# Optimization experiments

Measured on AMD Instinct MI355X. Metric: run time of the kernel, lower is better.

Reference implementation:

```python
import jax, jax.numpy as jnp
import numpy as np

B, L, D = 8, 2048, 64
EPS = 1e-8


def setup_inputs() -> dict:
    key = jax.random.key(0)
    ks = jax.random.split(key, 7)
    s = 1.0 / np.sqrt(D)  # ~ torch Linear default init scale
    return {
        "x": jax.random.normal(ks[0], (B, L, D), dtype=jnp.float32),
        "B_w": jax.random.normal(ks[1], (D, D), dtype=jnp.float32) * s,
        "B_b": jax.random.normal(ks[2], (D,), dtype=jnp.float32) * s,
        "C_w": jax.random.normal(ks[3], (D, D), dtype=jnp.float32) * s,
        "C_b": jax.random.normal(ks[4], (D,), dtype=jnp.float32) * s,
        "V_w": jax.random.normal(ks[5], (D, D), dtype=jnp.float32) * s,
        "V_b": jax.random.normal(ks[6], (D,), dtype=jnp.float32) * s,
    }


def reference(x, B_w, B_b, C_w, C_b, V_w, V_b):
    # torch nn.Linear: y = x @ W.T + b
    BZ = jnp.einsum('bld,ed->ble', x, B_w) + B_b   # (B,L,D)
    CZ = jnp.einsum('bld,ed->ble', x, C_w) + C_b   # (B,L,D)
    scores = jnp.einsum('bld,bmd->blm', BZ, CZ)     # (B,L,L)
    attn = jax.nn.relu(scores)
    # note: normalization over dim=-2 (column sums), as in the original
    attn = attn / (attn.sum(axis=-2, keepdims=True) + EPS)
    VZ = jnp.einsum('bld,ed->ble', x, V_w) + V_b   # (B,L,D)
    out = jnp.einsum('blm,bmd->bld', attn, VZ)      # (B,L,D)
    return x + out
```

## Files before the change

### kernel.cpp

```cpp
#include <hip/hip_runtime.h>

typedef unsigned short u16;
typedef unsigned int u32;
typedef __bf16 bf16x8 __attribute__((ext_vector_type(8)));
typedef float f32x16 __attribute__((ext_vector_type(16)));
typedef const void __attribute__((address_space(1))) gvoid;
typedef void __attribute__((address_space(3))) lvoid;

#define GLOAD16(gp, lp) __builtin_amdgcn_global_load_lds((gvoid*)(gp), (lvoid*)(lp), 16, 0, 0)
#define POST_BARRIER_FENCE() do { __builtin_amdgcn_sched_barrier(0); asm volatile("" ::: "memory"); } while (0)

namespace {
constexpr int Ln = 2048;
constexpr float EPS = 1e-8f;
}

__device__ __forceinline__ u32 pk2(float lo, float hi) {
    u32 r;
    asm("v_cvt_pk_bf16_f32 %0, %1, %2" : "=v"(r) : "v"(lo), "v"(hi));
    return r;
}

__device__ __forceinline__ void half_swap(u32 a, u32 b, u32& na, u32& nb) {
    u32 sa = (u32)__shfl_xor((int)a, 32, 64);
    u32 sb = (u32)__shfl_xor((int)b, 32, 64);
    int hi = (threadIdx.x & 63) >> 5;
    na = hi ? a : sb;
    nb = hi ? sa : b;
}

__global__ __launch_bounds__(128) void proj_k(
    const float* __restrict__ x,
    const float* __restrict__ Bw, const float* __restrict__ Bb,
    const float* __restrict__ Cw, const float* __restrict__ Cb,
    const float* __restrict__ Vw, const float* __restrict__ Vb,
    u16* __restrict__ BZh, u16* __restrict__ CZh, u16* __restrict__ VZTh)
{
    const int tid = threadIdx.x;
    const int ln = tid & 31;
    const int g5 = (tid >> 5) & 1;
    const int w  = tid >> 6;
    const int row0 = blockIdx.x * 64 + w * 32;

    bf16x8 wf[3][2][4];
    const float* const Wp[3] = {Bw, Cw, Vw};
    #pragma unroll
    for (int m = 0; m < 3; ++m)
      #pragma unroll
      for (int e = 0; e < 2; ++e)
        #pragma unroll
        for (int c = 0; c < 4; ++c) {
            const float* p = Wp[m] + (e * 32 + ln) * 64 + c * 16 + g5 * 8;
            const float4 lo = *(const float4*)p;
            const float4 hi = *(const float4*)(p + 4);
            uint4 t4;
            t4.x = pk2(lo.x, lo.y); t4.y = pk2(lo.z, lo.w);
            t4.z = pk2(hi.x, hi.y); t4.w = pk2(hi.z, hi.w);
            wf[m][e][c] = __builtin_bit_cast(bf16x8, t4);
        }
    bf16x8 xf[4];
    {
        const float* xp = x + (row0 + ln) * 64 + g5 * 8;
        #pragma unroll
        for (int c = 0; c < 4; ++c) {
            const float4 lo = *(const float4*)(xp + c * 16);
            const float4 hi = *(const float4*)(xp + c * 16 + 4);
            uint4 t4;
            t4.x = pk2(lo.x, lo.y); t4.y = pk2(lo.z, lo.w);
            t4.z = pk2(hi.x, hi.y); t4.w = pk2(hi.z, hi.w);
            xf[c] = __builtin_bit_cast(bf16x8, t4);
        }
    }
    const int b   = row0 >> 11;
    const int l0b = row0 & 2047;
    const float* const biasBC[2] = {Bb, Cb};
    u16* const outBC[2] = {BZh, CZh};
    #pragma unroll
    for (int m = 0; m < 2; ++m) {
        #pragma unroll
        for (int e = 0; e < 2; ++e) {
            f32x16 st;
            #pragma unroll
            for (int q = 0; q < 4; ++q) {
                const float4 bv = *(const float4*)(biasBC[m] + e * 32 + q * 8 + g5 * 4);
                st[q*4+0] = bv.x; st[q*4+1] = bv.y; st[q*4+2] = bv.z; st[q*4+3] = bv.w;
            }
            #pragma unroll
            for (int c = 0; c < 4; ++c)
                st = __builtin_amdgcn_mfma_f32_32x32x16_bf16(wf[m][e][c], xf[c], st, 0, 0, 0);
            u16* op = outBC[m] + (row0 + ln) * 64 + e * 32 + g5 * 4;
            #pragma unroll
            for (int q = 0; q < 4; ++q) {
                uint2 pk;
                pk.x = pk2(st[q*4+0], st[q*4+1]);
                pk.y = pk2(st[q*4+2], st[q*4+3]);
                *(uint2*)(op + q * 8) = pk;
            }
        }
    }
    #pragma unroll
    for (int e = 0; e < 2; ++e) {
        const float vb = Vb[e * 32 + ln];
        f32x16 st;
        #pragma unroll
        for (int r = 0; r < 16; ++r) st[r] = vb;
        #pragma unroll
        for (int c = 0; c < 4; ++c)
            st = __builtin_amdgcn_mfma_f32_32x32x16_bf16(xf[c], wf[2][e][c], st, 0, 0, 0);
        u16* op = VZTh + (b * 64 + e * 32 + ln) * Ln + l0b + g5 * 4;
        #pragma unroll
        for (int q = 0; q < 4; ++q) {
            uint2 pk;
            pk.x = pk2(st[q*4+0], st[q*4+1]);
            pk.y = pk2(st[q*4+2], st[q*4+3]);
            *(uint2*)(op + q * 8) = pk;
        }
    }
}

__global__ __launch_bounds__(512) void denom_k(
    const u16* __restrict__ BZh, const u16* __restrict__ CZh,
    float* __restrict__ denp)
{
    __shared__ __attribute__((aligned(16))) char smem2[49152 + 1024];
    float* const red = (float*)(smem2 + 49152);
    const int tid = threadIdx.x;
    const int lane = tid & 63;
    const int ln = lane & 31;
    const int g5 = lane >> 5;
    const int w = tid >> 6;
    const int wm2 = w & 1, wl2 = w >> 1;
    const int flat = (int)blockIdx.z * 256 + (int)blockIdx.y * 32 + (int)blockIdx.x;
    const int nf = (flat & 7) * 64 + (flat >> 3);
    const int b = nf >> 6;
    const int rem = nf & 63;
    const int mb = (rem & 31) * 64;
    const int half = rem >> 5;
    const int l0h = half * 1024;
    const int wave_base = tid & ~63;

    bf16x8 af[4];
    {
        const u16* cp = CZh + ((b * Ln + mb + wm2 * 32 + ln) << 6) + g5 * 8;
        #pragma unroll
        for (int c = 0; c < 4; ++c) af[c] = *(const bf16x8*)(cp + c * 16);
    }
    auto stageD = [&](int t) {
        char* buf = smem2 + (t % 3) * 16384;
        #pragma unroll
        for (int it = 0; it < 2; ++it) {
            int j = (it << 9) + tid;
            int r = j >> 3;
            int u = (j & 7) ^ (r & 7);
            GLOAD16(BZh + ((b * Ln + l0h + t * 128 + r) << 6) + (u << 3),
                    buf + ((it << 9) + wave_base) * 16);
        }
    };
    stageD(0); stageD(1);
    __syncthreads();
    float accs[16];
    #pragma unroll
    for (int r = 0; r < 16; ++r) accs[r] = 0.f;
    const int lr = wl2 * 32 + ln;
    for (int t = 0; t < 8; ++t) {
        if (t > 0) {
            if (t < 7) asm volatile("s_waitcnt vmcnt(2)" ::: "memory");
            else       asm volatile("s_waitcnt vmcnt(0)" ::: "memory");
            __builtin_amdgcn_s_barrier();
            POST_BARRIER_FENCE();
        }
        if (t + 2 < 8) stageD(t + 2);
        const char* buf = smem2 + (t % 3) * 16384;
        f32x16 st = {};
        __builtin_amdgcn_s_setprio(1);
        #pragma unroll
        for (int c = 0; c < 4; ++c) {
            int un = (c << 1) | g5;
            bf16x8 bfr = *(const bf16x8*)(buf + (lr << 7) + ((un ^ (lr & 7)) << 4));
            st = __builtin_amdgcn_mfma_f32_32x32x16_bf16(af[c], bfr, st, 0, 0, 0);
        }
        __builtin_amdgcn_s_setprio(0);
        #pragma unroll
        for (int r = 0; r < 16; ++r) accs[r] += fmaxf(st[r], 0.f);
    }
    #pragma unroll
    for (int msk = 1; msk <= 16; msk <<= 1)
        #pragma unroll
        for (int r = 0; r < 16; ++r)
            accs[r] += __shfl_xor(accs[r], msk, 64);
    if (ln == 0) {
        #pragma unroll
        for (int r = 0; r < 16; ++r) {
            int mloc = wm2 * 32 + (r & 3) + ((r >> 2) << 3) + g5 * 4;
            red[mloc * 4 + wl2] = accs[r];
        }
    }
    __syncthreads();
    if (tid < 64)
        denp[(half * 8 + b) * Ln + mb + tid] =
            red[tid*4+0] + red[tid*4+1] + red[tid*4+2] + red[tid*4+3];
}

__global__ __launch_bounds__(512) void fused_out(
    const float* __restrict__ x,
    const u16* __restrict__ BZh, const u16* __restrict__ CZh,
    const u16* __restrict__ VZTh, const float* __restrict__ denp,
    float* __restrict__ out)
{
    __shared__ __attribute__((aligned(16))) char smem[57344];
    float* const denl = (float*)smem;
    char* const bufs = smem + 8192;
    const int tid = threadIdx.x;
    const int lane = tid & 63;
    const int ln = lane & 31;
    const int g5 = lane >> 5;
    const int w = tid >> 6;
    const int wm = w & 3;
    const int wl = w >> 2;
    const int bx = (int)blockIdx.x;
    const int nf = (bx & 7) * 32 + (bx >> 3);
    const int b = nf >> 5;
    const int l0 = (nf & 31) * 64;
    const int wave_base = tid & ~63;

    auto stage = [&](int t) {
        char* vzb = bufs + (t % 3) * 16384;
        #pragma unroll
        for (int it = 0; it < 2; ++it) {
            int j = (it << 9) + tid;
            int r = j >> 4;
            int uu = (j & 15) ^ (r & 7);
            GLOAD16(VZTh + ((b << 6) + r) * Ln + (t << 7) + (uu << 3),
                    vzb + ((it << 9) + wave_base) * 16);
        }
    };
    const u16* const cp0 = CZh + ((b * Ln + wm * 32 + ln) << 6) + g5 * 8;
    auto loadA = [&](int t, bf16x8* dst) {
        const u16* p = cp0 + ((t * 128) << 6);
        #pragma unroll
        for (int c = 0; c < 4; ++c) dst[c] = *(const bf16x8*)(p + c * 16);
    };

    {
        const float4 c0 = *(const float4*)(denp + b * Ln + tid * 4);
        const float4 c1 = *(const float4*)(denp + (8 + b) * Ln + tid * 4);
        float4 dv;
        dv.x = 1.f / (c0.x + c1.x + EPS);
        dv.y = 1.f / (c0.y + c1.y + EPS);
        dv.z = 1.f / (c0.z + c1.z + EPS);
        dv.w = 1.f / (c0.w + c1.w + EPS);
        *(float4*)(denl + tid * 4) = dv;
    }
    bf16x8 bzf[4];
    {
        const u16* bp = BZh + ((b * Ln + l0 + wl * 32 + ln) << 6) + g5 * 8;
        #pragma unroll
        for (int c = 0; c < 4; ++c) bzf[c] = *(const bf16x8*)(bp + c * 16);
    }
    stage(0); stage(1);
    bf16x8 aF[2][4];
    loadA(0, aF[0]);
    __syncthreads();

    f32x16 acc0 = {}, acc1 = {};
    #pragma unroll
    for (int t = 0; t < 16; ++t) {
        const int cur = t & 1;
        if (t > 0) {
            __builtin_amdgcn_s_barrier();
            POST_BARRIER_FENCE();
        }
        if (t + 2 < 16) stage(t + 2);
        if (t + 1 < 16) loadA(t + 1, aF[cur ^ 1]);
        f32x16 st = {};
        __builtin_amdgcn_s_setprio(1);
        #pragma unroll
        for (int c = 0; c < 4; ++c)
            st = __builtin_amdgcn_mfma_f32_32x32x16_bf16(aF[cur][c], bzf[c], st, 0, 0, 0);
        __builtin_amdgcn_s_setprio(0);
        const int mq0 = (t << 7) + wm * 32;
        u32 wv[8];
        #pragma unroll
        for (int q = 0; q < 4; ++q) {
            const float4 dq = *(const float4*)(denl + mq0 + q * 8 + g5 * 4);
            float p0 = fmaxf(st[q*4+0], 0.f) * dq.x;
            float p1 = fmaxf(st[q*4+1], 0.f) * dq.y;
            float p2 = fmaxf(st[q*4+2], 0.f) * dq.z;
            float p3 = fmaxf(st[q*4+3], 0.f) * dq.w;
            wv[q*2+0] = pk2(p0, p1);
            wv[q*2+1] = pk2(p2, p3);
        }
        u32 f0w0, f0w1, f0w2, f0w3, f1w0, f1w1, f1w2, f1w3;
        half_swap(wv[2], wv[0], f0w2, f0w0);
        half_swap(wv[3], wv[1], f0w3, f0w1);
        half_swap(wv[6], wv[4], f1w2, f1w0);
        half_swap(wv[7], wv[5], f1w3, f1w1);
        bf16x8 pf0, pf1;
        { uint4 t4; t4.x=f0w0; t4.y=f0w1; t4.z=f0w2; t4.w=f0w3; pf0 = __builtin_bit_cast(bf16x8, t4); }
        { uint4 t4; t4.x=f1w0; t4.y=f1w1; t4.z=f1w2; t4.w=f1w3; pf1 = __builtin_bit_cast(bf16x8, t4); }
        const char* vz = bufs + (t % 3) * 16384;
        const int un00 = (wm << 2) | g5;
        const int un01 = (wm << 2) | 2 | g5;
        __builtin_amdgcn_s_setprio(1);
        {
            bf16x8 av;
            av = *(const bf16x8*)(vz + (ln << 8) + ((un00 ^ (ln & 7)) << 4));
            acc0 = __builtin_amdgcn_mfma_f32_32x32x16_bf16(av, pf0, acc0, 0, 0, 0);
            av = *(const bf16x8*)(vz + (ln << 8) + ((un01 ^ (ln & 7)) << 4));
            acc0 = __builtin_amdgcn_mfma_f32_32x32x16_bf16(av, pf1, acc0, 0, 0, 0);
            av = *(const bf16x8*)(vz + ((32 + ln) << 8) + ((un00 ^ (ln & 7)) << 4));
            acc1 = __builtin_amdgcn_mfma_f32_32x32x16_bf16(av, pf0, acc1, 0, 0, 0);
            av = *(const bf16x8*)(vz + ((32 + ln) << 8) + ((un01 ^ (ln & 7)) << 4));
            acc1 = __builtin_amdgcn_mfma_f32_32x32x16_bf16(av, pf1, acc1, 0, 0, 0);
        }
        __builtin_amdgcn_s_setprio(0);
    }

    __syncthreads();
    float* red = (float*)smem;
    constexpr int LSTR = 36;
    constexpr int SSTR = 64 * LSTR;
    if (wm != 0) {
        float* base = red + ((wm - 1) * 2 + wl) * SSTR + lane * LSTR;
        #pragma unroll
        for (int r = 0; r < 16; ++r) { base[r] = acc0[r]; base[16 + r] = acc1[r]; }
    }
    __syncthreads();
    if (wm == 0) {
        #pragma unroll
        for (int s = 0; s < 3; ++s) {
            float* base = red + (s * 2 + wl) * SSTR + lane * LSTR;
            #pragma unroll
            for (int r = 0; r < 16; ++r) { acc0[r] += base[r]; acc1[r] += base[16 + r]; }
        }
        const int row = b * Ln + l0 + wl * 32 + ln;
        #pragma unroll
        for (int q = 0; q < 4; ++q) {
            const int d0 = q * 8 + g5 * 4;
            const float4 x0 = *(const float4*)(x + row * 64 + d0);
            float4 o0;
            o0.x = x0.x + acc0[q*4+0]; o0.y = x0.y + acc0[q*4+1];
            o0.z = x0.z + acc0[q*4+2]; o0.w = x0.w + acc0[q*4+3];
            *(float4*)(out + row * 64 + d0) = o0;
            const float4 x1 = *(const float4*)(x + row * 64 + 32 + d0);
            float4 o1;
            o1.x = x1.x + acc1[q*4+0]; o1.y = x1.y + acc1[q*4+1];
            o1.z = x1.z + acc1[q*4+2]; o1.w = x1.w + acc1[q*4+3];
            *(float4*)(out + row * 64 + 32 + d0) = o1;
        }
    }
}

extern "C" void kernel_launch(void* const* d_in, const int* in_sizes, int n_in,
                              void* d_out, int out_size, void* d_ws, size_t ws_size,
                              hipStream_t stream) {
    const float* x  = (const float*)d_in[0];
    const float* Bw = (const float*)d_in[1];
    const float* Bb = (const float*)d_in[2];
    const float* Cw = (const float*)d_in[3];
    const float* Cb = (const float*)d_in[4];
    const float* Vw = (const float*)d_in[5];
    const float* Vb = (const float*)d_in[6];
    float* out = (float*)d_out;
    char* wsb = (char*)d_ws;
    u16* BZh  = (u16*)wsb;
    u16* CZh  = (u16*)(wsb + (2u << 20));
    u16* VZTh = (u16*)(wsb + (4u << 20));
    float* denp = (float*)(wsb + (6u << 20));

    proj_k<<<dim3(256), 128, 0, stream>>>(x, Bw, Bb, Cw, Cb, Vw, Vb, BZh, CZh, VZTh);
    denom_k<<<dim3(32, 8, 2), 512, 0, stream>>>(BZh, CZh, denp);
    fused_out<<<dim3(256), 512, 0, stream>>>(x, BZh, CZh, VZTh, denp, out);
}
```

Before: 56.57 us.

## Restructure fused_out to stage CZ and VZ via LDS in 256-wide m tiles

The fused output kernel now has each of 8 waves own a 32-row m slice and all 64 l rows, instead of splitting waves over l halves and m quarters. CZ tiles are now staged into LDS with async global-to-LDS loads alongside VZ, double-buffered in 256-column chunks, which halves the loop trips and reuses each CZ fragment for two score tiles. The cross-wave reduction becomes a three-step tree over 8 waves, and proj_k is relaunched as 128 blocks of 256 threads. This raises LDS use to about 136KB per block, which limits occupancy to one block per CU, and adds a full vmcnt wait before each barrier.

```diff
diff --git a/kernel.cpp b/kernel.cpp
--- a/kernel.cpp
+++ b/kernel.cpp
@@ -29,7 +29,7 @@
     nb = hi ? sa : b;
 }
 
-__global__ __launch_bounds__(128) void proj_k(
+__global__ __launch_bounds__(256) void proj_k(
     const float* __restrict__ x,
     const float* __restrict__ Bw, const float* __restrict__ Bb,
     const float* __restrict__ Cw, const float* __restrict__ Cb,
@@ -40,7 +40,7 @@
     const int ln = tid & 31;
     const int g5 = (tid >> 5) & 1;
     const int w  = tid >> 6;
-    const int row0 = blockIdx.x * 64 + w * 32;
+    const int row0 = blockIdx.x * 128 + w * 32;
 
     bf16x8 wf[3][2][4];
     const float* const Wp[3] = {Bw, Cw, Vw};
@@ -207,16 +207,14 @@
     const u16* __restrict__ VZTh, const float* __restrict__ denp,
     float* __restrict__ out)
 {
-    __shared__ __attribute__((aligned(16))) char smem[57344];
+    __shared__ __attribute__((aligned(16))) char smem[139264];
     float* const denl = (float*)smem;
     char* const bufs = smem + 8192;
     const int tid = threadIdx.x;
     const int lane = tid & 63;
     const int ln = lane & 31;
     const int g5 = lane >> 5;
-    const int w = tid >> 6;
-    const int wm = w & 3;
-    const int wl = w >> 2;
+    const int wm = tid >> 6;
     const int bx = (int)blockIdx.x;
     const int nf = (bx & 7) * 32 + (bx >> 3);
     const int b = nf >> 5;
@@ -224,23 +222,28 @@
     const int wave_base = tid & ~63;
 
     auto stage = [&](int t) {
-        char* vzb = bufs + (t % 3) * 16384;
-        #pragma unroll
-        for (int it = 0; it < 2; ++it) {
+        char* czb = bufs + (t & 1) * 65536;
+        char* vzb = czb + 32768;
+        const int m0s = t << 8;
+        #pragma unroll
+        for (int it = 0; it < 4; ++it) {
             int j = (it << 9) + tid;
-            int r = j >> 4;
-            int uu = (j & 15) ^ (r & 7);
-            GLOAD16(VZTh + ((b << 6) + r) * Ln + (t << 7) + (uu << 3),
+            int r = j >> 3;
+            int u = (j & 7) ^ (r & 7);
+            GLOAD16(CZh + ((b * Ln + m0s + r) << 6) + (u << 3),
+                    czb + ((it << 9) + wave_base) * 16);
+        }
+        #pragma unroll
+        for (int it = 0; it < 4; ++it) {
+            int j = (it << 9) + tid;
+            int r = j >> 5;
+            int u = (j & 31) ^ (r & 7);
+            GLOAD16(VZTh + ((b << 6) + r) * Ln + m0s + (u << 3),
                     vzb + ((it << 9) + wave_base) * 16);
         }
     };
-    const u16* const cp0 = CZh + ((b * Ln + wm * 32 + ln) << 6) + g5 * 8;
-    auto loadA = [&](int t, bf16x8* dst) {
-        const u16* p = cp0 + ((t * 128) << 6);
-        #pragma unroll
-        for (int c = 0; c < 4; ++c) dst[c] = *(const bf16x8*)(p + c * 16);
-    };
-
+
+    stage(0);
     {
         const float4 c0 = *(const float4*)(denp + b * Ln + tid * 4);
         const float4 c1 = *(const float4*)(denp + (8 + b) * Ln + tid * 4);
@@ -251,102 +254,166 @@
         dv.w = 1.f / (c0.w + c1.w + EPS);
         *(float4*)(denl + tid * 4) = dv;
     }
-    bf16x8 bzf[4];
+    bf16x8 bzf0[4], bzf1[4];
     {
-        const u16* bp = BZh + ((b * Ln + l0 + wl * 32 + ln) << 6) + g5 * 8;
-        #pragma unroll
-        for (int c = 0; c < 4; ++c) bzf[c] = *(const bf16x8*)(bp + c * 16);
-    }
-    stage(0); stage(1);
-    bf16x8 aF[2][4];
-    loadA(0, aF[0]);
-    __syncthreads();
-
-    f32x16 acc0 = {}, acc1 = {};
-    #pragma unroll
-    for (int t = 0; t < 16; ++t) {
-        const int cur = t & 1;
+        const u16* bp0 = BZh + ((b * Ln + l0 + ln) << 6) + g5 * 8;
+        const u16* bp1 = BZh + ((b * Ln + l0 + 32 + ln) << 6) + g5 * 8;
+        #pragma unroll
+        for (int c = 0; c < 4; ++c) {
+            bzf0[c] = *(const bf16x8*)(bp0 + c * 16);
+            bzf1[c] = *(const bf16x8*)(bp1 + c * 16);
+        }
+    }
+    __syncthreads();
+
+    f32x16 acc00 = {}, acc01 = {}, acc10 = {}, acc11 = {};
+    const int mr = wm * 32 + ln;
+
+    for (int t = 0; t < 8; ++t) {
         if (t > 0) {
+            asm volatile("s_waitcnt vmcnt(0)" ::: "memory");
             __builtin_amdgcn_s_barrier();
             POST_BARRIER_FENCE();
         }
-        if (t + 2 < 16) stage(t + 2);
-        if (t + 1 < 16) loadA(t + 1, aF[cur ^ 1]);
-        f32x16 st = {};
-        __builtin_amdgcn_s_setprio(1);
-        #pragma unroll
-        for (int c = 0; c < 4; ++c)
-            st = __builtin_amdgcn_mfma_f32_32x32x16_bf16(aF[cur][c], bzf[c], st, 0, 0, 0);
-        __builtin_amdgcn_s_setprio(0);
-        const int mq0 = (t << 7) + wm * 32;
-        u32 wv[8];
-        #pragma unroll
-        for (int q = 0; q < 4; ++q) {
-            const float4 dq = *(const float4*)(denl + mq0 + q * 8 + g5 * 4);
-            float p0 = fmaxf(st[q*4+0], 0.f) * dq.x;
-            float p1 = fmaxf(st[q*4+1], 0.f) * dq.y;
-            float p2 = fmaxf(st[q*4+2], 0.f) * dq.z;
-            float p3 = fmaxf(st[q*4+3], 0.f) * dq.w;
-            wv[q*2+0] = pk2(p0, p1);
-            wv[q*2+1] = pk2(p2, p3);
-        }
-        u32 f0w0, f0w1, f0w2, f0w3, f1w0, f1w1, f1w2, f1w3;
-        half_swap(wv[2], wv[0], f0w2, f0w0);
-        half_swap(wv[3], wv[1], f0w3, f0w1);
-        half_swap(wv[6], wv[4], f1w2, f1w0);
-        half_swap(wv[7], wv[5], f1w3, f1w1);
-        bf16x8 pf0, pf1;
-        { uint4 t4; t4.x=f0w0; t4.y=f0w1; t4.z=f0w2; t4.w=f0w3; pf0 = __builtin_bit_cast(bf16x8, t4); }
-        { uint4 t4; t4.x=f1w0; t4.y=f1w1; t4.z=f1w2; t4.w=f1w3; pf1 = __builtin_bit_cast(bf16x8, t4); }
-        const char* vz = bufs + (t % 3) * 16384;
-        const int un00 = (wm << 2) | g5;
-        const int un01 = (wm << 2) | 2 | g5;
-        __builtin_amdgcn_s_setprio(1);
+        if (t + 1 < 8) stage(t + 1);
+        const char* czb = bufs + (t & 1) * 65536;
+        const char* vzb = czb + 32768;
+        bf16x8 a0, a1, a2, a3;
         {
-            bf16x8 av;
-            av = *(const bf16x8*)(vz + (ln << 8) + ((un00 ^ (ln & 7)) << 4));
-            acc0 = __builtin_amdgcn_mfma_f32_32x32x16_bf16(av, pf0, acc0, 0, 0, 0);
-            av = *(const bf16x8*)(vz + (ln << 8) + ((un01 ^ (ln & 7)) << 4));
-            acc0 = __builtin_amdgcn_mfma_f32_32x32x16_bf16(av, pf1, acc0, 0, 0, 0);
-            av = *(const bf16x8*)(vz + ((32 + ln) << 8) + ((un00 ^ (ln & 7)) << 4));
-            acc1 = __builtin_amdgcn_mfma_f32_32x32x16_bf16(av, pf0, acc1, 0, 0, 0);
-            av = *(const bf16x8*)(vz + ((32 + ln) << 8) + ((un01 ^ (ln & 7)) << 4));
-            acc1 = __builtin_amdgcn_mfma_f32_32x32x16_bf16(av, pf1, acc1, 0, 0, 0);
-        }
-        __builtin_amdgcn_s_setprio(0);
-    }
-
-    __syncthreads();
-    float* red = (float*)smem;
-    constexpr int LSTR = 36;
+            const char* base = czb + (mr << 7);
+            a0 = *(const bf16x8*)(base + (((0 | g5) ^ (mr & 7)) << 4));
+            a1 = *(const bf16x8*)(base + (((2 | g5) ^ (mr & 7)) << 4));
+            a2 = *(const bf16x8*)(base + (((4 | g5) ^ (mr & 7)) << 4));
+            a3 = *(const bf16x8*)(base + (((6 | g5) ^ (mr & 7)) << 4));
+        }
+        const int mq0 = (t << 8) + wm * 32;
+        bf16x8 pf0h0, pf1h0, pf0h1, pf1h1;
+        {
+            f32x16 st = {};
+            __builtin_amdgcn_s_setprio(1);
+            st = __builtin_amdgcn_mfma_f32_32x32x16_bf16(a0, bzf0[0], st, 0, 0, 0);
+            st = __builtin_amdgcn_mfma_f32_32x32x16_bf16(a1, bzf0[1], st, 0, 0, 0);
+            st = __builtin_amdgcn_mfma_f32_32x32x16_bf16(a2, bzf0[2], st, 0, 0, 0);
+            st = __builtin_amdgcn_mfma_f32_32x32x16_bf16(a3, bzf0[3], st, 0, 0, 0);
+            __builtin_amdgcn_s_setprio(0);
+            u32 wv[8];
+            #pragma unroll
+            for (int q = 0; q < 4; ++q) {
+                const float4 dq = *(const float4*)(denl + mq0 + q * 8 + g5 * 4);
+                float p0 = fmaxf(st[q*4+0], 0.f) * dq.x;
+                float p1 = fmaxf(st[q*4+1], 0.f) * dq.y;
+                float p2 = fmaxf(st[q*4+2], 0.f) * dq.z;
+                float p3 = fmaxf(st[q*4+3], 0.f) * dq.w;
+                wv[q*2+0] = pk2(p0, p1);
+                wv[q*2+1] = pk2(p2, p3);
+            }
+            u32 f0w0, f0w1, f0w2, f0w3, f1w0, f1w1, f1w2, f1w3;
+            half_swap(wv[2], wv[0], f0w2, f0w0);
+            half_swap(wv[3], wv[1], f0w3, f0w1);
+            half_swap(wv[6], wv[4], f1w2, f1w0);
+            half_swap(wv[7], wv[5], f1w3, f1w1);
+            { uint4 t4; t4.x=f0w0; t4.y=f0w1; t4.z=f0w2; t4.w=f0w3; pf0h0 = __builtin_bit_cast(bf16x8, t4); }
+            { uint4 t4; t4.x=f1w0; t4.y=f1w1; t4.z=f1w2; t4.w=f1w3; pf1h0 = __builtin_bit_cast(bf16x8, t4); }
+        }
+        {
+            f32x16 st = {};
+            __builtin_amdgcn_s_setprio(1);
+            st = __builtin_amdgcn_mfma_f32_32x32x16_bf16(a0, bzf1[0], st, 0, 0, 0);
+            st = __builtin_amdgcn_mfma_f32_32x32x16_bf16(a1, bzf1[1], st, 0, 0, 0);
+            st = __builtin_amdgcn_mfma_f32_32x32x16_bf16(a2, bzf1[2], st, 0, 0, 0);
+            st = __builtin_amdgcn_mfma_f32_32x32x16_bf16(a3, bzf1[3], st, 0, 0, 0);
+            __builtin_amdgcn_s_setprio(0);
+            u32 wv[8];
+            #pragma unroll
+            for (int q = 0; q < 4; ++q) {
+                const float4 dq = *(const float4*)(denl + mq0 + q * 8 + g5 * 4);
+                float p0 = fmaxf(st[q*4+0], 0.f) * dq.x;
+                float p1 = fmaxf(st[q*4+1], 0.f) * dq.y;
+                float p2 = fmaxf(st[q*4+2], 0.f) * dq.z;
+                float p3 = fmaxf(st[q*4+3], 0.f) * dq.w;
+                wv[q*2+0] = pk2(p0, p1);
+                wv[q*2+1] = pk2(p2, p3);
+            }
+            u32 f0w0, f0w1, f0w2, f0w3, f1w0, f1w1, f1w2, f1w3;
+            half_swap(wv[2], wv[0], f0w2, f0w0);
+            half_swap(wv[3], wv[1], f0w3, f0w1);
+            half_swap(wv[6], wv[4], f1w2, f1w0);
+            half_swap(wv[7], wv[5], f1w3, f1w1);
+            { uint4 t4; t4.x=f0w0; t4.y=f0w1; t4.z=f0w2; t4.w=f0w3; pf0h1 = __builtin_bit_cast(bf16x8, t4); }
+            { uint4 t4; t4.x=f1w0; t4.y=f1w1; t4.z=f1w2; t4.w=f1w3; pf1h1 = __builtin_bit_cast(bf16x8, t4); }
+        }
+        {
+            const int un0 = (wm << 2) | g5;
+            const int un1 = (wm << 2) | 2 | g5;
+            const char* r0 = vzb + (ln << 9);
+            const char* r1 = vzb + ((32 + ln) << 9);
+            bf16x8 av00 = *(const bf16x8*)(r0 + ((un0 ^ (ln & 7)) << 4));
+            bf16x8 av01 = *(const bf16x8*)(r0 + ((un1 ^ (ln & 7)) << 4));
+            bf16x8 av10 = *(const bf16x8*)(r1 + ((un0 ^ (ln & 7)) << 4));
+            bf16x8 av11 = *(const bf16x8*)(r1 + ((un1 ^ (ln & 7)) << 4));
+            __builtin_amdgcn_s_setprio(1);
+            acc00 = __builtin_amdgcn_mfma_f32_32x32x16_bf16(av00, pf0h0, acc00, 0, 0, 0);
+            acc00 = __builtin_amdgcn_mfma_f32_32x32x16_bf16(av01, pf1h0, acc00, 0, 0, 0);
+            acc01 = __builtin_amdgcn_mfma_f32_32x32x16_bf16(av00, pf0h1, acc01, 0, 0, 0);
+            acc01 = __builtin_amdgcn_mfma_f32_32x32x16_bf16(av01, pf1h1, acc01, 0, 0, 0);
+            acc10 = __builtin_amdgcn_mfma_f32_32x32x16_bf16(av10, pf0h0, acc10, 0, 0, 0);
+            acc10 = __builtin_amdgcn_mfma_f32_32x32x16_bf16(av11, pf1h0, acc10, 0, 0, 0);
+            acc11 = __builtin_amdgcn_mfma_f32_32x32x16_bf16(av10, pf0h1, acc11, 0, 0, 0);
+            acc11 = __builtin_amdgcn_mfma_f32_32x32x16_bf16(av11, pf1h1, acc11, 0, 0, 0);
+            __builtin_amdgcn_s_setprio(0);
+        }
+    }
+
+    __syncthreads();
+    float* red = (float*)bufs;
+    constexpr int LSTR = 68;
     constexpr int SSTR = 64 * LSTR;
-    if (wm != 0) {
-        float* base = red + ((wm - 1) * 2 + wl) * SSTR + lane * LSTR;
-        #pragma unroll
-        for (int r = 0; r < 16; ++r) { base[r] = acc0[r]; base[16 + r] = acc1[r]; }
-    }
+    auto wslot = [&](int s) { return red + s * SSTR + lane * LSTR; };
+    auto put = [&](float* p) {
+        #pragma unroll
+        for (int r = 0; r < 16; ++r) {
+            p[r]      = acc00[r]; p[16 + r] = acc01[r];
+            p[32 + r] = acc10[r]; p[48 + r] = acc11[r];
+        }
+    };
+    auto add = [&](const float* p) {
+        #pragma unroll
+        for (int r = 0; r < 16; ++r) {
+            acc00[r] += p[r];      acc01[r] += p[16 + r];
+            acc10[r] += p[32 + r]; acc11[r] += p[48 + r];
+        }
+    };
+    if (wm >= 4) put(wslot(wm - 4));
+    __syncthreads();
+    if (wm < 4) add(wslot(wm));
+    __syncthreads();
+    if (wm == 2 || wm == 3) put(wslot(wm - 2));
+    __syncthreads();
+    if (wm < 2) add(wslot(wm));
+    __syncthreads();
+    if (wm == 1) put(wslot(0));
     __syncthreads();
     if (wm == 0) {
-        #pragma unroll
-        for (int s = 0; s < 3; ++s) {
-            float* base = red + (s * 2 + wl) * SSTR + lane * LSTR;
-            #pragma unroll
-            for (int r = 0; r < 16; ++r) { acc0[r] += base[r]; acc1[r] += base[16 + r]; }
-        }
-        const int row = b * Ln + l0 + wl * 32 + ln;
-        #pragma unroll
-        for (int q = 0; q < 4; ++q) {
-            const int d0 = q * 8 + g5 * 4;
-            const float4 x0 = *(const float4*)(x + row * 64 + d0);
-            float4 o0;
-            o0.x = x0.x + acc0[q*4+0]; o0.y = x0.y + acc0[q*4+1];
-            o0.z = x0.z + acc0[q*4+2]; o0.w = x0.w + acc0[q*4+3];
-            *(float4*)(out + row * 64 + d0) = o0;
-            const float4 x1 = *(const float4*)(x + row * 64 + 32 + d0);
-            float4 o1;
-            o1.x = x1.x + acc1[q*4+0]; o1.y = x1.y + acc1[q*4+1];
-            o1.z = x1.z + acc1[q*4+2]; o1.w = x1.w + acc1[q*4+3];
-            *(float4*)(out + row * 64 + 32 + d0) = o1;
+        add(wslot(0));
+        #pragma unroll
+        for (int h = 0; h < 2; ++h) {
+            const int row = b * Ln + l0 + h * 32 + ln;
+            #pragma unroll
+            for (int q = 0; q < 4; ++q) {
+                const int d0 = q * 8 + g5 * 4;
+                const f32x16& alo = h ? acc01 : acc00;
+                const f32x16& ahi = h ? acc11 : acc10;
+                const float4 x0 = *(const float4*)(x + row * 64 + d0);
+                float4 o0;
+                o0.x = x0.x + alo[q*4+0]; o0.y = x0.y + alo[q*4+1];
+                o0.z = x0.z + alo[q*4+2]; o0.w = x0.w + alo[q*4+3];
+                *(float4*)(out + row * 64 + d0) = o0;
+                const float4 x1 = *(const float4*)(x + row * 64 + 32 + d0);
+                float4 o1;
+                o1.x = x1.x + ahi[q*4+0]; o1.y = x1.y + ahi[q*4+1];
+                o1.z = x1.z + ahi[q*4+2]; o1.w = x1.w + ahi[q*4+3];
+                *(float4*)(out + row * 64 + 32 + d0) = o1;
+            }
         }
     }
 }
@@ -368,7 +435,7 @@
     u16* VZTh = (u16*)(wsb + (4u << 20));
     float* denp = (float*)(wsb + (6u << 20));
 
-    proj_k<<<dim3(256), 128, 0, stream>>>(x, Bw, Bb, Cw, Cb, Vw, Vb, BZh, CZh, VZTh);
+    proj_k<<<dim3(128), 256, 0, stream>>>(x, Bw, Bb, Cw, Cb, Vw, Vb, BZh, CZh, VZTh);
     denom_k<<<dim3(32, 8, 2), 512, 0, stream>>>(BZh, CZh, denp);
     fused_out<<<dim3(256), 512, 0, stream>>>(x, BZh, CZh, VZTh, denp, out);
 }
```

After: 51.00 us. 1.11x faster.

## Stage CZ tiles through LDS with double buffering and tree-reduce partials

Applied to the files above, without the earlier changes.

In fused_out, CZ tiles are now staged into LDS with global_load_lds alongside the VZ^T tiles. The old per-wave register prefetch of CZ is gone, and the triple-buffered VZ ring becomes a double-buffered CZ+VZ pair with a full vmcnt(0) wait each iteration. The cross-wave reduction becomes a two-level tree, and launch bounds gain a min-blocks hint of 4. The aim is to share CZ loads across waves instead of having each wave read them from global memory, and to shorten the serial reduction. In exchange, LDS use grows to 72KB per block, prefetch depth drops to one stage, and the main loop is no longer unrolled.

```diff
diff --git a/kernel.cpp b/kernel.cpp
--- a/kernel.cpp
+++ b/kernel.cpp
@@ -41,6 +41,8 @@
     const int g5 = (tid >> 5) & 1;
     const int w  = tid >> 6;
     const int row0 = blockIdx.x * 64 + w * 32;
+    const int b   = row0 >> 11;
+    const int l0b = row0 & 2047;
 
     bf16x8 wf[3][2][4];
     const float* const Wp[3] = {Bw, Cw, Vw};
@@ -71,8 +73,6 @@
             xf[c] = __builtin_bit_cast(bf16x8, t4);
         }
     }
-    const int b   = row0 >> 11;
-    const int l0b = row0 & 2047;
     const float* const biasBC[2] = {Bb, Cb};
     u16* const outBC[2] = {BZh, CZh};
     #pragma unroll
@@ -138,6 +138,7 @@
     const int half = rem >> 5;
     const int l0h = half * 1024;
     const int wave_base = tid & ~63;
+    const int lr = wl2 * 32 + ln;
 
     bf16x8 af[4];
     {
@@ -161,7 +162,6 @@
     float accs[16];
     #pragma unroll
     for (int r = 0; r < 16; ++r) accs[r] = 0.f;
-    const int lr = wl2 * 32 + ln;
     for (int t = 0; t < 8; ++t) {
         if (t > 0) {
             if (t < 7) asm volatile("s_waitcnt vmcnt(2)" ::: "memory");
@@ -201,13 +201,13 @@
             red[tid*4+0] + red[tid*4+1] + red[tid*4+2] + red[tid*4+3];
 }
 
-__global__ __launch_bounds__(512) void fused_out(
+__global__ __launch_bounds__(512, 4) void fused_out(
     const float* __restrict__ x,
     const u16* __restrict__ BZh, const u16* __restrict__ CZh,
     const u16* __restrict__ VZTh, const float* __restrict__ denp,
     float* __restrict__ out)
 {
-    __shared__ __attribute__((aligned(16))) char smem[57344];
+    __shared__ __attribute__((aligned(16))) char smem[73728];
     float* const denl = (float*)smem;
     char* const bufs = smem + 8192;
     const int tid = threadIdx.x;
@@ -222,25 +222,31 @@
     const int b = nf >> 5;
     const int l0 = (nf & 31) * 64;
     const int wave_base = tid & ~63;
+    const int mA = wm * 32 + ln;
 
     auto stage = [&](int t) {
-        char* vzb = bufs + (t % 3) * 16384;
+        char* bufc = bufs + (t & 1) * 32768;
+        char* vzb = bufc + 16384;
+        const int m0s = t << 7;
+        #pragma unroll
+        for (int it = 0; it < 2; ++it) {
+            int j = (it << 9) + tid;
+            int r = j >> 3;
+            int u = (j & 7) ^ (r & 7);
+            GLOAD16(CZh + ((b * Ln + m0s + r) << 6) + (u << 3),
+                    bufc + ((it << 9) + wave_base) * 16);
+        }
         #pragma unroll
         for (int it = 0; it < 2; ++it) {
             int j = (it << 9) + tid;
             int r = j >> 4;
-            int uu = (j & 15) ^ (r & 7);
-            GLOAD16(VZTh + ((b << 6) + r) * Ln + (t << 7) + (uu << 3),
+            int u = (j & 15) ^ (r & 7);
+            GLOAD16(VZTh + ((b << 6) + r) * Ln + m0s + (u << 3),
                     vzb + ((it << 9) + wave_base) * 16);
         }
     };
-    const u16* const cp0 = CZh + ((b * Ln + wm * 32 + ln) << 6) + g5 * 8;
-    auto loadA = [&](int t, bf16x8* dst) {
-        const u16* p = cp0 + ((t * 128) << 6);
-        #pragma unroll
-        for (int c = 0; c < 4; ++c) dst[c] = *(const bf16x8*)(p + c * 16);
-    };
-
+
+    stage(0);
     {
         const float4 c0 = *(const float4*)(denp + b * Ln + tid * 4);
         const float4 c1 = *(const float4*)(denp + (8 + b) * Ln + tid * 4);
@@ -257,26 +263,26 @@
         #pragma unroll
         for (int c = 0; c < 4; ++c) bzf[c] = *(const bf16x8*)(bp + c * 16);
     }
-    stage(0); stage(1);
-    bf16x8 aF[2][4];
-    loadA(0, aF[0]);
     __syncthreads();
 
     f32x16 acc0 = {}, acc1 = {};
-    #pragma unroll
     for (int t = 0; t < 16; ++t) {
-        const int cur = t & 1;
         if (t > 0) {
+            asm volatile("s_waitcnt vmcnt(0)" ::: "memory");
             __builtin_amdgcn_s_barrier();
             POST_BARRIER_FENCE();
         }
-        if (t + 2 < 16) stage(t + 2);
-        if (t + 1 < 16) loadA(t + 1, aF[cur ^ 1]);
+        if (t + 1 < 16) stage(t + 1);
+        const char* cz = bufs + (t & 1) * 32768;
+        const char* vz = cz + 16384;
         f32x16 st = {};
         __builtin_amdgcn_s_setprio(1);
         #pragma unroll
-        for (int c = 0; c < 4; ++c)
-            st = __builtin_amdgcn_mfma_f32_32x32x16_bf16(aF[cur][c], bzf[c], st, 0, 0, 0);
+        for (int c = 0; c < 4; ++c) {
+            int un = (c << 1) | g5;
+            bf16x8 a = *(const bf16x8*)(cz + (mA << 7) + ((un ^ (mA & 7)) << 4));
+            st = __builtin_amdgcn_mfma_f32_32x32x16_bf16(a, bzf[c], st, 0, 0, 0);
+        }
         __builtin_amdgcn_s_setprio(0);
         const int mq0 = (t << 7) + wm * 32;
         u32 wv[8];
@@ -298,7 +304,6 @@
         bf16x8 pf0, pf1;
         { uint4 t4; t4.x=f0w0; t4.y=f0w1; t4.z=f0w2; t4.w=f0w3; pf0 = __builtin_bit_cast(bf16x8, t4); }
         { uint4 t4; t4.x=f1w0; t4.y=f1w1; t4.z=f1w2; t4.w=f1w3; pf1 = __builtin_bit_cast(bf16x8, t4); }
-        const char* vz = bufs + (t % 3) * 16384;
         const int un00 = (wm << 2) | g5;
         const int un01 = (wm << 2) | 2 | g5;
         __builtin_amdgcn_s_setprio(1);
@@ -317,22 +322,31 @@
     }
 
     __syncthreads();
-    float* red = (float*)smem;
+    float* red = (float*)bufs;
     constexpr int LSTR = 36;
     constexpr int SSTR = 64 * LSTR;
-    if (wm != 0) {
-        float* base = red + ((wm - 1) * 2 + wl) * SSTR + lane * LSTR;
+    if (wm >= 2) {
+        float* base = red + (wl * 2 + (wm - 2)) * SSTR + lane * LSTR;
         #pragma unroll
         for (int r = 0; r < 16; ++r) { base[r] = acc0[r]; base[16 + r] = acc1[r]; }
     }
     __syncthreads();
+    if (wm < 2) {
+        float* base = red + (wl * 2 + wm) * SSTR + lane * LSTR;
+        #pragma unroll
+        for (int r = 0; r < 16; ++r) { acc0[r] += base[r]; acc1[r] += base[16 + r]; }
+    }
+    __syncthreads();
+    if (wm == 1) {
+        float* base = red + (4 + wl) * SSTR + lane * LSTR;
+        #pragma unroll
+        for (int r = 0; r < 16; ++r) { base[r] = acc0[r]; base[16 + r] = acc1[r]; }
+    }
+    __syncthreads();
     if (wm == 0) {
-        #pragma unroll
-        for (int s = 0; s < 3; ++s) {
-            float* base = red + (s * 2 + wl) * SSTR + lane * LSTR;
-            #pragma unroll
-            for (int r = 0; r < 16; ++r) { acc0[r] += base[r]; acc1[r] += base[16 + r]; }
-        }
+        float* base = red + (4 + wl) * SSTR + lane * LSTR;
+        #pragma unroll
+        for (int r = 0; r < 16; ++r) { acc0[r] += base[r]; acc1[r] += base[16 + r]; }
         const int row = b * Ln + l0 + wl * 32 + ln;
         #pragma unroll
         for (int q = 0; q < 4; ++q) {
```

Result: faster. 47.97 us (-15.2%).
